# Kernel optimization log

Measured on AMD Instinct MI355X. Metric: run time of the kernel, lower is better.

## Reference

```python
import jax, jax.numpy as jnp
import numpy as np

B = 65536          # number of 17-node circle graphs in the batch
NN = 17            # nodes per graph (hardcoded in module)
FEAT = 32          # feature_num


def _circle_edge_index(num_graphs):
    s = np.arange(NN)
    d = (s + 1) % NN
    src0 = np.concatenate([s, d])   # bidirectional ring
    dst0 = np.concatenate([d, s])
    off = (np.arange(num_graphs) * NN)[:, None]
    src = (src0[None, :] + off).ravel()
    dst = (dst0[None, :] + off).ravel()
    return jnp.asarray(np.stack([src, dst]).astype(np.int32))


def setup_inputs() -> dict:
    key = jax.random.key(0)
    ks = jax.random.split(key, 10)
    p = lambda k, shp, fan: jax.random.normal(k, shp, jnp.float32) / np.sqrt(fan)
    return {
        "z": jax.random.normal(ks[0], (B, FEAT), jnp.float32),
        "edge_index": _circle_edge_index(B),                      # [2, 2*17*B]
        "fc_w": p(ks[1], (FEAT, NN * 8), FEAT),
        "fc_b": jnp.zeros((NN * 8,), jnp.float32),
        "w1": p(ks[2], (8, 16), 8),
        "b1": jnp.zeros((16,), jnp.float32),
        "w2": p(ks[3], (16, 32), 16),
        "b2": jnp.zeros((32,), jnp.float32),
        "w3": p(ks[4], (32, FEAT), 32),
        "b3": jnp.zeros((FEAT,), jnp.float32),
    }


def _gcn(x, src, tgt, norm, W, b, n_nodes):
    # GCNConv: out[t] = sum_{(s,t)} norm(s,t) * (x[s] @ W) + b
    h = x @ W
    msg = h[src] * norm[:, None]
    return jax.ops.segment_sum(msg, tgt, num_segments=n_nodes) + b


def reference(z, edge_index, fc_w, fc_b, w1, b1, w2, b2, w3, b3):
    n_nodes = z.shape[0] * NN
    # fc_expand then reshape to node features [N, 8]
    x = (z @ fc_w + fc_b).reshape(-1, 8)
    # symmetric GCN normalization with added self-loops (same for all 3 convs)
    loop = jnp.arange(n_nodes, dtype=edge_index.dtype)
    src = jnp.concatenate([edge_index[0], loop])
    tgt = jnp.concatenate([edge_index[1], loop])
    deg = jax.ops.segment_sum(jnp.ones_like(tgt, dtype=x.dtype), tgt,
                              num_segments=n_nodes)
    dinv = jax.lax.rsqrt(deg)  # deg >= 1 because of self-loops
    norm = dinv[src] * dinv[tgt]
    x = jax.nn.relu(_gcn(x, src, tgt, norm, w1, b1, n_nodes))
    x = jax.nn.relu(_gcn(x, src, tgt, norm, w2, b2, n_nodes))
    x = _gcn(x, src, tgt, norm, w3, b3, n_nodes)
    return x.reshape(-1, NN, FEAT)
```

## Files before the change

kernel.cpp:

```cpp
#include <hip/hip_runtime.h>
#include <stdint.h>

typedef unsigned short u16;
typedef unsigned int   u32;
typedef __attribute__((ext_vector_type(8))) short bf16x8;
typedef __attribute__((ext_vector_type(4))) float f32x4;

#define NN   17
#define G    16
#define ROWS (G*NN)
#define TPB  256
#define XS1  24
#define XS2  40

__device__ u16   g_w1p_frag[NN*512];
__device__ float g_b1p[ROWS];
__device__ u16   g_w2_frag[2*512];
__device__ u16   g_w3_frag[2*512];
__device__ float g_bias2[32];
__device__ float g_bias3[32];

__device__ __forceinline__ float uf(u32 u){ union{u32 a; float b;} c; c.a=u; return c.b; }
__device__ __forceinline__ u32   fu(float f){ union{float a; u32 b;} c; c.a=f; return c.b; }
__device__ __forceinline__ u16 f2bf(float f){
    u32 u = fu(f);
    return (u16)((u + 0x7FFFu + ((u >> 16) & 1u)) >> 16);
}
__device__ __forceinline__ bf16x8 as_bf16x8(uint4 v){ union{uint4 a; bf16x8 b;} c; c.a=v; return c.b; }

__device__ __forceinline__ u32 cvtpk(float lo, float hi){
    u32 r; asm("v_cvt_pk_bf16_f32 %0, %1, %2" : "=v"(r) : "v"(lo), "v"(hi)); return r;
}

__device__ __forceinline__ u32 ringsum3_pk(u32 a, u32 b, u32 c){
    const u32 M = 0xFFFF0000u;
    float hs = uf(a & M) + uf(b & M) + uf(c & M);
    float ls = uf(a << 16) + uf(b << 16) + uf(c << 16);
    return cvtpk(ls, hs);
}

__global__ void gnn_prep(const float* __restrict__ fcw, const float* __restrict__ fcb,
                         const float* __restrict__ w1,  const float* __restrict__ b1,
                         const float* __restrict__ w2,  const float* __restrict__ b2,
                         const float* __restrict__ w3,  const float* __restrict__ b3)
{
    const int t = threadIdx.x, blk = blockIdx.x;
    const float inv3 = 1.0f/3.0f;

    if (blk < NN) {
        __shared__ float s_avg[32][8];
        __shared__ float s_w1[8][16];
        const int i  = blk;
        const int im = (i == 0    ? NN-1 : i-1);
        const int ip = (i == NN-1 ? 0    : i+1);
        {   int k = t >> 3, f = t & 7;
            s_avg[k][f] = (fcw[k*136 + im*8+f] + fcw[k*136 + i*8+f] + fcw[k*136 + ip*8+f]) * inv3;
        }
        if (t < 128) s_w1[t >> 4][t & 15] = w1[t];
        __syncthreads();
        for (int e = t; e < 512; e += TPB) {
            int ln = e >> 3, j = e & 7;
            int k = (ln >> 4)*8 + j, c = ln & 15;
            float v = 0.f;
            #pragma unroll
            for (int f = 0; f < 8; ++f) v += s_avg[k][f] * s_w1[f][c];
            g_w1p_frag[i*512 + e] = f2bf(v);
        }
    } else {
        for (int e = t; e < 1024; e += TPB) {
            int h = e >> 9, ln = (e >> 3) & 63, j = e & 7;
            int k = (ln >> 4)*8 + j, c = 2*(ln & 15) + h;
            g_w2_frag[e] = (k < 16) ? f2bf(w2[k*32 + c] * inv3) : (u16)0;
            g_w3_frag[e] = f2bf(w3[k*32 + c] * inv3);
        }
        if (t < 32) { g_bias2[t] = b2[t]; g_bias3[t] = b3[t]; }
        for (int e = t; e < ROWS; e += TPB) {
            int i = e >> 4, c = e & 15;
            int im = (i == 0    ? NN-1 : i-1);
            int ip = (i == NN-1 ? 0    : i+1);
            float v = b1[c];
            #pragma unroll
            for (int f = 0; f < 8; ++f)
                v += (fcb[im*8+f] + fcb[i*8+f] + fcb[ip*8+f]) * inv3 * w1[f*16 + c];
            g_b1p[e] = v;
        }
    }
}

__global__ __launch_bounds__(TPB, 4)
void gnn_main(const float* __restrict__ z, float* __restrict__ out, int nG)
{
    __shared__ __align__(16) u16 x1[ROWS*XS1];
    __shared__ __align__(16) u16 x2[ROWS*XS2];

    const int t = threadIdx.x, wv = t >> 6, ln = t & 63;
    const int quad = ln >> 4, l16 = ln & 15;
    int gmax = nG - blockIdx.x * G; if (gmax > G) gmax = G;

    bf16x8 fw1t[5]; float b1v[5];
    #pragma unroll
    for (int s = 0; s < 5; ++s) {
        int tile = wv + 4*s;
        if (tile < NN) {
            fw1t[s] = *(const bf16x8*)(g_w1p_frag + tile*512 + ln*8);
            b1v[s]  = g_b1p[tile*16 + l16];
        } else { fw1t[s] = (bf16x8){0,0,0,0,0,0,0,0}; b1v[s] = 0.f; }
    }
    bf16x8 fw2e = *(const bf16x8*)(g_w2_frag + ln*8);
    bf16x8 fw2o = *(const bf16x8*)(g_w2_frag + 512 + ln*8);
    bf16x8 fw3e = *(const bf16x8*)(g_w3_frag + ln*8);
    bf16x8 fw3o = *(const bf16x8*)(g_w3_frag + 512 + ln*8);
    const float b2e = g_bias2[2*l16], b2o = g_bias2[2*l16+1];
    const float b3e = g_bias3[2*l16], b3o = g_bias3[2*l16+1];

    bf16x8 az = (bf16x8){0,0,0,0,0,0,0,0};
    if (l16 < gmax) {
        const float* zp = z + ((size_t)blockIdx.x*G + l16)*32 + quad*8;
        float4 a0 = *(const float4*)zp, a1 = *(const float4*)(zp + 4);
        az = as_bf16x8(make_uint4(cvtpk(a0.x,a0.y), cvtpk(a0.z,a0.w),
                                  cvtpk(a1.x,a1.y), cvtpk(a1.z,a1.w)));
    }

    #pragma unroll
    for (int s = 0; s < 5; ++s) {
        int tile = wv + 4*s;
        if (tile < NN) {
            f32x4 cb = {b1v[s], b1v[s], b1v[s], b1v[s]};
            f32x4 d = __builtin_amdgcn_mfma_f32_16x16x32_bf16(az, fw1t[s], cb, 0, 0, 0);
            u32 p01 = cvtpk(fmaxf(d[0],0.f), fmaxf(d[1],0.f));
            u32 p23 = cvtpk(fmaxf(d[2],0.f), fmaxf(d[3],0.f));
            int base = ((quad*4)*NN + tile)*XS1 + l16;
            x1[base]              = (u16)p01;
            x1[base +   NN*XS1]   = (u16)(p01 >> 16);
            x1[base + 2*NN*XS1]   = (u16)p23;
            x1[base + 3*NN*XS1]   = (u16)(p23 >> 16);
        }
    }
    __syncthreads();

    {
        f32x4 cbe = {b2e,b2e,b2e,b2e}, cbo = {b2o,b2o,b2o,b2o};
        u32* ob2 = (u32*)x2;
        #pragma unroll
        for (int s = 0; s < 5; ++s) {
            int tile = wv + 4*s;
            if (tile < NN) {
                bf16x8 af = (bf16x8){0,0,0,0,0,0,0,0};
                if (quad < 2) {
                    int rr = tile*16 + l16;
                    int gg = (rr*3856) >> 16; int i = rr - gg*NN;
                    int rm = rr + (i == 0    ? NN-1 : -1);
                    int rp = rr + (i == NN-1 ? 1-NN  :  1);
                    uint4 A  = *(const uint4*)&x1[rm*XS1 + quad*8];
                    uint4 Bv = *(const uint4*)&x1[rr*XS1 + quad*8];
                    uint4 Cv = *(const uint4*)&x1[rp*XS1 + quad*8];
                    af = as_bf16x8(make_uint4(ringsum3_pk(A.x,Bv.x,Cv.x), ringsum3_pk(A.y,Bv.y,Cv.y),
                                              ringsum3_pk(A.z,Bv.z,Cv.z), ringsum3_pk(A.w,Bv.w,Cv.w)));
                }
                f32x4 d0 = __builtin_amdgcn_mfma_f32_16x16x32_bf16(af, fw2e, cbe, 0, 0, 0);
                f32x4 d1 = __builtin_amdgcn_mfma_f32_16x16x32_bf16(af, fw2o, cbo, 0, 0, 0);
                #pragma unroll
                for (int r = 0; r < 4; ++r) {
                    int rr2 = tile*16 + quad*4 + r;
                    ob2[rr2*(XS2/2) + l16] = cvtpk(fmaxf(d0[r],0.f), fmaxf(d1[r],0.f));
                }
            }
        }
    }
    __syncthreads();

    {
        f32x4 cbe = {b3e,b3e,b3e,b3e}, cbo = {b3o,b3o,b3o,b3o};
        float* ob = out + (size_t)blockIdx.x * (ROWS*32);
        const int rowmax = gmax * NN;
        #pragma unroll
        for (int s = 0; s < 5; ++s) {
            int tile = wv + 4*s;
            if (tile < NN) {
                int rr = tile*16 + l16;
                int gg = (rr*3856) >> 16; int i = rr - gg*NN;
                int rm = rr + (i == 0    ? NN-1 : -1);
                int rp = rr + (i == NN-1 ? 1-NN  :  1);
                uint4 A  = *(const uint4*)&x2[rm*XS2 + quad*8];
                uint4 Bv = *(const uint4*)&x2[rr*XS2 + quad*8];
                uint4 Cv = *(const uint4*)&x2[rp*XS2 + quad*8];
                bf16x8 af = as_bf16x8(make_uint4(ringsum3_pk(A.x,Bv.x,Cv.x), ringsum3_pk(A.y,Bv.y,Cv.y),
                                                 ringsum3_pk(A.z,Bv.z,Cv.z), ringsum3_pk(A.w,Bv.w,Cv.w)));
                f32x4 d0 = __builtin_amdgcn_mfma_f32_16x16x32_bf16(af, fw3e, cbe, 0, 0, 0);
                f32x4 d1 = __builtin_amdgcn_mfma_f32_16x16x32_bf16(af, fw3o, cbo, 0, 0, 0);
                #pragma unroll
                for (int r = 0; r < 4; ++r) {
                    int rr2 = tile*16 + quad*4 + r;
                    if (rr2 < rowmax) {
                        float2 v = make_float2(d0[r], d1[r]);
                        *(float2*)&ob[(size_t)rr2*32 + 2*l16] = v;
                    }
                }
            }
        }
    }
}

extern "C" void kernel_launch(void* const* d_in, const int* in_sizes, int n_in,
                              void* d_out, int out_size, void* d_ws, size_t ws_size,
                              hipStream_t stream) {
    const float* z    = (const float*)d_in[0];
    const float* fcw  = (const float*)d_in[2];
    const float* fcb  = (const float*)d_in[3];
    const float* w1   = (const float*)d_in[4];
    const float* b1   = (const float*)d_in[5];
    const float* w2   = (const float*)d_in[6];
    const float* b2   = (const float*)d_in[7];
    const float* w3   = (const float*)d_in[8];
    const float* b3   = (const float*)d_in[9];
    float* out = (float*)d_out;

    const int nG   = in_sizes[0] / 32;
    const int grid = (nG + G - 1) / G;
    gnn_prep<<<NN + 1, TPB, 0, stream>>>(fcw, fcb, w1, b1, w2, b2, w3, b3);
    gnn_main<<<grid, TPB, 0, stream>>>(z, out, nG);
}
```

Baseline: 187.2 us.

## Transpose MFMA operands so outputs land row-contiguous, with XOR-swizzled LDS

Swaps the A and B operands of every MFMA so each lane holds four consecutive feature columns of one node row. Node activations can then be written to LDS as packed 8-byte stores, and the final output as 16-byte float4 stores instead of scattered 16-bit and float2 writes. The padded LDS strides are replaced by dense buffers with XOR swizzles to avoid bank conflicts. Bias vectors are loaded as f32x4 per lane, and launch bounds rise to 5 blocks per CU to raise occupancy, at the risk of register pressure and a predicate that now covers the MFMA as well.

```diff
diff --git a/kernel.cpp b/kernel.cpp
--- a/kernel.cpp
+++ b/kernel.cpp
@@ -10,15 +10,14 @@
 #define G    16
 #define ROWS (G*NN)
 #define TPB  256
-#define XS1  24
-#define XS2  40
-
-__device__ u16   g_w1p_frag[NN*512];
-__device__ float g_b1p[ROWS];
-__device__ u16   g_w2_frag[2*512];
-__device__ u16   g_w3_frag[2*512];
-__device__ float g_bias2[32];
-__device__ float g_bias3[32];
+
+
+__device__ __align__(16) u16   g_w1p_frag[NN*512];
+__device__ __align__(16) float g_b1p[ROWS];
+__device__ __align__(16) u16   g_w2_frag[2*512];
+__device__ __align__(16) u16   g_w3_frag[2*512];
+__device__ __align__(16) float g_bias2[32];
+__device__ __align__(16) float g_bias3[32];
 
 __device__ __forceinline__ float uf(u32 u){ union{u32 a; float b;} c; c.a=u; return c.b; }
 __device__ __forceinline__ u32   fu(float f){ union{float a; u32 b;} c; c.a=f; return c.b; }
@@ -69,7 +68,7 @@
     } else {
         for (int e = t; e < 1024; e += TPB) {
             int h = e >> 9, ln = (e >> 3) & 63, j = e & 7;
-            int k = (ln >> 4)*8 + j, c = 2*(ln & 15) + h;
+            int k = (ln >> 4)*8 + j, c = h*16 + (ln & 15);
             g_w2_frag[e] = (k < 16) ? f2bf(w2[k*32 + c] * inv3) : (u16)0;
             g_w3_frag[e] = f2bf(w3[k*32 + c] * inv3);
         }
@@ -87,31 +86,31 @@
     }
 }
 
-__global__ __launch_bounds__(TPB, 4)
+__global__ __launch_bounds__(TPB, 5)
 void gnn_main(const float* __restrict__ z, float* __restrict__ out, int nG)
 {
-    __shared__ __align__(16) u16 x1[ROWS*XS1];
-    __shared__ __align__(16) u16 x2[ROWS*XS2];
+    __shared__ __align__(16) u32 x1[ROWS*8];
+    __shared__ __align__(16) u32 x2[ROWS*16];
 
     const int t = threadIdx.x, wv = t >> 6, ln = t & 63;
     const int quad = ln >> 4, l16 = ln & 15;
     int gmax = nG - blockIdx.x * G; if (gmax > G) gmax = G;
 
-    bf16x8 fw1t[5]; float b1v[5];
+    bf16x8 fw1t[5];
     #pragma unroll
     for (int s = 0; s < 5; ++s) {
         int tile = wv + 4*s;
-        if (tile < NN) {
-            fw1t[s] = *(const bf16x8*)(g_w1p_frag + tile*512 + ln*8);
-            b1v[s]  = g_b1p[tile*16 + l16];
-        } else { fw1t[s] = (bf16x8){0,0,0,0,0,0,0,0}; b1v[s] = 0.f; }
-    }
-    bf16x8 fw2e = *(const bf16x8*)(g_w2_frag + ln*8);
-    bf16x8 fw2o = *(const bf16x8*)(g_w2_frag + 512 + ln*8);
-    bf16x8 fw3e = *(const bf16x8*)(g_w3_frag + ln*8);
-    bf16x8 fw3o = *(const bf16x8*)(g_w3_frag + 512 + ln*8);
-    const float b2e = g_bias2[2*l16], b2o = g_bias2[2*l16+1];
-    const float b3e = g_bias3[2*l16], b3o = g_bias3[2*l16+1];
+        fw1t[s] = (tile < NN) ? *(const bf16x8*)(g_w1p_frag + tile*512 + ln*8)
+                              : (bf16x8){0,0,0,0,0,0,0,0};
+    }
+    bf16x8 fw2[2], fw3[2]; f32x4 cb2[2], cb3[2];
+    #pragma unroll
+    for (int h = 0; h < 2; ++h) {
+        fw2[h] = *(const bf16x8*)(g_w2_frag + h*512 + ln*8);
+        fw3[h] = *(const bf16x8*)(g_w3_frag + h*512 + ln*8);
+        cb2[h] = *(const f32x4*)(g_bias2 + h*16 + quad*4);
+        cb3[h] = *(const f32x4*)(g_bias3 + h*16 + quad*4);
+    }
 
     bf16x8 az = (bf16x8){0,0,0,0,0,0,0,0};
     if (l16 < gmax) {
@@ -125,52 +124,47 @@
     for (int s = 0; s < 5; ++s) {
         int tile = wv + 4*s;
         if (tile < NN) {
-            f32x4 cb = {b1v[s], b1v[s], b1v[s], b1v[s]};
-            f32x4 d = __builtin_amdgcn_mfma_f32_16x16x32_bf16(az, fw1t[s], cb, 0, 0, 0);
+            f32x4 cb1 = *(const f32x4*)(g_b1p + tile*16 + quad*4);
+            f32x4 d = __builtin_amdgcn_mfma_f32_16x16x32_bf16(fw1t[s], az, cb1, 0, 0, 0);
             u32 p01 = cvtpk(fmaxf(d[0],0.f), fmaxf(d[1],0.f));
             u32 p23 = cvtpk(fmaxf(d[2],0.f), fmaxf(d[3],0.f));
-            int base = ((quad*4)*NN + tile)*XS1 + l16;
-            x1[base]              = (u16)p01;
-            x1[base +   NN*XS1]   = (u16)(p01 >> 16);
-            x1[base + 2*NN*XS1]   = (u16)p23;
-            x1[base + 3*NN*XS1]   = (u16)(p23 >> 16);
+            int row = l16*NN + tile;
+            int idx = (row*8 + quad*2) ^ (((row >> 2) & 1) << 2);
+            *(uint2*)&x1[idx] = make_uint2(p01, p23);
         }
     }
     __syncthreads();
 
+    #pragma unroll
+    for (int s = 0; s < 5; ++s) {
+        int tile = wv + 4*s;
+        if (tile < NN) {
+            int rr = tile*16 + l16;
+            bf16x8 af = (bf16x8){0,0,0,0,0,0,0,0};
+            if (quad < 2) {
+                int gg = (rr*3856) >> 16; int i = rr - gg*NN;
+                int rm = rr + (i == 0    ? NN-1 : -1);
+                int rp = rr + (i == NN-1 ? 1-NN  :  1);
+                uint4 A  = *(const uint4*)&x1[(rm*8 + quad*4) ^ (((rm >> 2) & 1) << 2)];
+                uint4 Bv = *(const uint4*)&x1[(rr*8 + quad*4) ^ (((rr >> 2) & 1) << 2)];
+                uint4 Cv = *(const uint4*)&x1[(rp*8 + quad*4) ^ (((rp >> 2) & 1) << 2)];
+                af = as_bf16x8(make_uint4(ringsum3_pk(A.x,Bv.x,Cv.x), ringsum3_pk(A.y,Bv.y,Cv.y),
+                                          ringsum3_pk(A.z,Bv.z,Cv.z), ringsum3_pk(A.w,Bv.w,Cv.w)));
+            }
+            int swz = ((rr >> 1) & 3) << 2;
+            #pragma unroll
+            for (int h = 0; h < 2; ++h) {
+                f32x4 d = __builtin_amdgcn_mfma_f32_16x16x32_bf16(fw2[h], af, cb2[h], 0, 0, 0);
+                u32 w0 = cvtpk(fmaxf(d[0],0.f), fmaxf(d[1],0.f));
+                u32 w1_ = cvtpk(fmaxf(d[2],0.f), fmaxf(d[3],0.f));
+                int idx = (rr*16 + h*8 + quad*2) ^ swz;
+                *(uint2*)&x2[idx] = make_uint2(w0, w1_);
+            }
+        }
+    }
+    __syncthreads();
+
     {
-        f32x4 cbe = {b2e,b2e,b2e,b2e}, cbo = {b2o,b2o,b2o,b2o};
-        u32* ob2 = (u32*)x2;
-        #pragma unroll
-        for (int s = 0; s < 5; ++s) {
-            int tile = wv + 4*s;
-            if (tile < NN) {
-                bf16x8 af = (bf16x8){0,0,0,0,0,0,0,0};
-                if (quad < 2) {
-                    int rr = tile*16 + l16;
-                    int gg = (rr*3856) >> 16; int i = rr - gg*NN;
-                    int rm = rr + (i == 0    ? NN-1 : -1);
-                    int rp = rr + (i == NN-1 ? 1-NN  :  1);
-                    uint4 A  = *(const uint4*)&x1[rm*XS1 + quad*8];
-                    uint4 Bv = *(const uint4*)&x1[rr*XS1 + quad*8];
-                    uint4 Cv = *(const uint4*)&x1[rp*XS1 + quad*8];
-                    af = as_bf16x8(make_uint4(ringsum3_pk(A.x,Bv.x,Cv.x), ringsum3_pk(A.y,Bv.y,Cv.y),
-                                              ringsum3_pk(A.z,Bv.z,Cv.z), ringsum3_pk(A.w,Bv.w,Cv.w)));
-                }
-                f32x4 d0 = __builtin_amdgcn_mfma_f32_16x16x32_bf16(af, fw2e, cbe, 0, 0, 0);
-                f32x4 d1 = __builtin_amdgcn_mfma_f32_16x16x32_bf16(af, fw2o, cbo, 0, 0, 0);
-                #pragma unroll
-                for (int r = 0; r < 4; ++r) {
-                    int rr2 = tile*16 + quad*4 + r;
-                    ob2[rr2*(XS2/2) + l16] = cvtpk(fmaxf(d0[r],0.f), fmaxf(d1[r],0.f));
-                }
-            }
-        }
-    }
-    __syncthreads();
-
-    {
-        f32x4 cbe = {b3e,b3e,b3e,b3e}, cbo = {b3o,b3o,b3o,b3o};
         float* ob = out + (size_t)blockIdx.x * (ROWS*32);
         const int rowmax = gmax * NN;
         #pragma unroll
@@ -181,19 +175,16 @@
                 int gg = (rr*3856) >> 16; int i = rr - gg*NN;
                 int rm = rr + (i == 0    ? NN-1 : -1);
                 int rp = rr + (i == NN-1 ? 1-NN  :  1);
-                uint4 A  = *(const uint4*)&x2[rm*XS2 + quad*8];
-                uint4 Bv = *(const uint4*)&x2[rr*XS2 + quad*8];
-                uint4 Cv = *(const uint4*)&x2[rp*XS2 + quad*8];
+                uint4 A  = *(const uint4*)&x2[(rm*16 + quad*4) ^ (((rm >> 1) & 3) << 2)];
+                uint4 Bv = *(const uint4*)&x2[(rr*16 + quad*4) ^ (((rr >> 1) & 3) << 2)];
+                uint4 Cv = *(const uint4*)&x2[(rp*16 + quad*4) ^ (((rp >> 1) & 3) << 2)];
                 bf16x8 af = as_bf16x8(make_uint4(ringsum3_pk(A.x,Bv.x,Cv.x), ringsum3_pk(A.y,Bv.y,Cv.y),
                                                  ringsum3_pk(A.z,Bv.z,Cv.z), ringsum3_pk(A.w,Bv.w,Cv.w)));
-                f32x4 d0 = __builtin_amdgcn_mfma_f32_16x16x32_bf16(af, fw3e, cbe, 0, 0, 0);
-                f32x4 d1 = __builtin_amdgcn_mfma_f32_16x16x32_bf16(af, fw3o, cbo, 0, 0, 0);
-                #pragma unroll
-                for (int r = 0; r < 4; ++r) {
-                    int rr2 = tile*16 + quad*4 + r;
-                    if (rr2 < rowmax) {
-                        float2 v = make_float2(d0[r], d1[r]);
-                        *(float2*)&ob[(size_t)rr2*32 + 2*l16] = v;
+                if (rr < rowmax) {
+                    #pragma unroll
+                    for (int h = 0; h < 2; ++h) {
+                        f32x4 d = __builtin_amdgcn_mfma_f32_16x16x32_bf16(fw3[h], af, cb3[h], 0, 0, 0);
+                        *(f32x4*)&ob[(size_t)rr*32 + h*16 + quad*4] = d;
                     }
                 }
             }
```

Result: no change. 190.5 us (+1.7%).
